# Kernel tuning notes

Measured on AMD Instinct MI355X. Metric: run time of the kernel, lower is better.

The kernel has to match this reference:

```python
import jax, jax.numpy as jnp
import numpy as np

N = 16384
E = 524288
D_IN = 256
D_OUT = 256


def setup_inputs() -> dict:
    key = jax.random.key(0)
    k1, k2, k3, k4, k5, k6 = jax.random.split(key, 6)
    x = jax.random.normal(k1, (N, D_IN), dtype=jnp.float32)
    edge_index = jax.random.randint(k2, (2, E), 0, N, dtype=jnp.int64)
    W_update = jax.random.normal(k3, (D_OUT, D_IN), dtype=jnp.float32) / np.sqrt(D_IN)
    b_update = jax.random.normal(k4, (D_OUT,), dtype=jnp.float32) * 0.01
    W_aggregate = jax.random.normal(k5, (D_OUT, D_IN), dtype=jnp.float32) / np.sqrt(D_IN)
    b_aggregate = jax.random.normal(k6, (D_OUT,), dtype=jnp.float32) * 0.01
    return {
        "x": x,
        "edge_index": edge_index,
        "W_update": W_update,
        "b_update": b_update,
        "W_aggregate": W_aggregate,
        "b_aggregate": b_aggregate,
    }


def reference(x, edge_index, W_update, b_update, W_aggregate, b_aggregate):
    n = x.shape[0]
    src, dst = edge_index[0], edge_index[1]
    # Dense symmetric 0/1 adjacency built with SET semantics (duplicate edges
    # contribute 1, not their count) -- faithful to the torch indexing assign.
    adj = jnp.zeros((n, n), dtype=x.dtype)
    adj = adj.at[src, dst].set(1.0)
    adj = adj.at[dst, src].set(1.0)
    messages = adj @ x                                   # [N, D_in]
    aggregated = messages @ W_aggregate.T + b_aggregate  # [N, D_out]
    updated = x @ W_update.T + b_update + aggregated     # [N, D_out]
    return updated
```

## Files before the change

### kernel.cpp

```cpp
#include <hip/hip_runtime.h>
#include <hip/hip_fp16.h>

#define NN 16384
#define DD 256
#define CAP 160
#define NB 128
#define BK 64
#define LDAP 72

typedef __attribute__((ext_vector_type(8))) __bf16 bf16x8;
typedef __attribute__((ext_vector_type(4))) float f32x4;

__device__ __forceinline__ unsigned short f2bn(float f) {
    __bf16 h = (__bf16)f;
    return __builtin_bit_cast(unsigned short, h);
}

__global__ __launch_bounds__(512) void k_hist(const int* __restrict__ ei,
                                              unsigned short* __restrict__ H,
                                              const float* __restrict__ Wu,
                                              const float* __restrict__ Wa,
                                              unsigned short* __restrict__ wb,
                                              int E, int epb) {
    const int b = blockIdx.x;
    const int t = threadIdx.x;

    if (b >= NB) {
        const int w = b - NB;
        const float* src = (w < 4) ? Wu : Wa;
        unsigned short* dst = wb + ((w < 4) ? 0 : 65536);
        const int c0 = (w & 3) * 4096;
#pragma unroll
        for (int i = 0; i < 8; ++i) {
            const int f4 = c0 + i * 512 + t;
            float4 v = *(const float4*)(src + (size_t)f4 * 4);
            ushort4 o;
            o.x = f2bn(v.x); o.y = f2bn(v.y); o.z = f2bn(v.z); o.w = f2bn(v.w);
            *(ushort4*)(dst + (size_t)f4 * 4) = o;
        }
        return;
    }

    __shared__ unsigned int h[NN / 2];
    for (int i = t; i < NN / 2; i += 512) h[i] = 0u;
    __syncthreads();

    const int e0 = b * epb;
    const int e1 = min(e0 + epb, E);
    for (int e = e0 + t; e < e1; e += 512) {
        const int s = ei[e];
        const int d = ei[E + e];
        atomicAdd(&h[s >> 1], 1u << ((s & 1) << 4));
        atomicAdd(&h[d >> 1], 1u << ((d & 1) << 4));
    }
    __syncthreads();

    unsigned short* Hb = H + (size_t)b * NN;
    for (int r = t; r < NN; r += 512)
        Hb[r] = (unsigned short)((h[r >> 1] >> ((r & 1) << 4)) & 0xffffu);
}

__global__ __launch_bounds__(512) void k_gemm_scan(const float* __restrict__ x,
                                                   const unsigned short* __restrict__ wb,
                                                   const float* __restrict__ bu,
                                                   const float* __restrict__ ba,
                                                   unsigned short* __restrict__ H,
                                                   unsigned int* __restrict__ cnt,
                                                   float* __restrict__ out,
                                                   __half* __restrict__ xab) {
    __shared__ __align__(16) unsigned short As[128 * LDAP];
    __shared__ __align__(16) unsigned short Bs[256 * LDAP];

    const int t = threadIdx.x;

    if (blockIdx.x >= 256) {
        const int r = (blockIdx.x - 256) * 512 + t;
        unsigned int base = 0;
#pragma unroll 8
        for (int bb = 0; bb < NB; ++bb) {
            const size_t a = (size_t)bb * NN + r;
            const unsigned int v = H[a];
            H[a] = (unsigned short)base;
            base += v;
        }
        cnt[r] = base;
        return;
    }

    const int lane = t & 63;
    const int wid = t >> 6;
    const int wr = wid >> 2;
    const int wc = wid & 3;
    const int row0 = (blockIdx.x >> 1) << 7;
    const int colp = blockIdx.x & 1;
    const unsigned short* Wsrc = wb + ((size_t)colp << 16);

    f32x4 acc[4][4] = {};

    for (int k0 = 0; k0 < DD; k0 += BK) {
        float4 ga[4];
        uint4 rb[4];
#pragma unroll
        for (int i = 0; i < 4; ++i) {
            const int ca = i * 512 + t;
            const int ar = ca >> 4, as = ca & 15;
            ga[i] = *(const float4*)(x + (size_t)(row0 + ar) * DD + k0 + as * 4);
            const int cb = i * 512 + t;
            const int br = cb >> 3, bs = cb & 7;
            rb[i] = *(const uint4*)(Wsrc + (size_t)br * DD + k0 + bs * 8);
        }
        __syncthreads();
#pragma unroll
        for (int i = 0; i < 4; ++i) {
            const int ca = i * 512 + t;
            const int ar = ca >> 4, as = ca & 15;
            ushort4 ap;
            ap.x = f2bn(ga[i].x); ap.y = f2bn(ga[i].y);
            ap.z = f2bn(ga[i].z); ap.w = f2bn(ga[i].w);
            *(ushort4*)(&As[ar * LDAP + as * 4]) = ap;
            const int cb = i * 512 + t;
            const int br = cb >> 3, bs = cb & 7;
            *(uint4*)(&Bs[br * LDAP + bs * 8]) = rb[i];
        }
        __syncthreads();
#pragma unroll
        for (int kk = 0; kk < 2; ++kk) {
            bf16x8 av[4], bv[4];
#pragma unroll
            for (int f = 0; f < 4; ++f) {
                uint4 ra = *(const uint4*)(&As[(wr * 64 + f * 16 + (lane & 15)) * LDAP + kk * 32 + (lane >> 4) * 8]);
                av[f] = __builtin_bit_cast(bf16x8, ra);
                uint4 rv = *(const uint4*)(&Bs[(wc * 64 + f * 16 + (lane & 15)) * LDAP + kk * 32 + (lane >> 4) * 8]);
                bv[f] = __builtin_bit_cast(bf16x8, rv);
            }
#pragma unroll
            for (int fm = 0; fm < 4; ++fm)
#pragma unroll
                for (int fn = 0; fn < 4; ++fn)
                    acc[fm][fn] = __builtin_amdgcn_mfma_f32_16x16x32_bf16(
                        av[fm], bv[fn], acc[fm][fn], 0, 0, 0);
        }
    }

    const int gr0 = row0 + wr * 64 + ((lane >> 4) << 2);
    const int gc0 = wc * 64 + (lane & 15);
    if (colp == 0) {
#pragma unroll
        for (int fn = 0; fn < 4; ++fn) {
            const int c = gc0 + fn * 16;
            const float bias = bu[c] + ba[c];
#pragma unroll
            for (int fm = 0; fm < 4; ++fm) {
                const int r = gr0 + fm * 16;
#pragma unroll
                for (int i = 0; i < 4; ++i)
                    out[(size_t)(r + i) * DD + c] = acc[fm][fn][i] + bias;
            }
        }
    } else {
#pragma unroll
        for (int fn = 0; fn < 4; ++fn) {
            const int c = gc0 + fn * 16;
#pragma unroll
            for (int fm = 0; fm < 4; ++fm) {
                const int r = gr0 + fm * 16;
#pragma unroll
                for (int i = 0; i < 4; ++i)
                    xab[(size_t)(r + i) * DD + c] = __float2half(acc[fm][fn][i]);
            }
        }
    }
}

__global__ __launch_bounds__(512) void k_fill(const int* __restrict__ ei,
                                              const unsigned short* __restrict__ H,
                                              unsigned short* __restrict__ list,
                                              int E, int epb) {
    __shared__ unsigned int off[NN / 2];
    const int b = blockIdx.x;
    const int t = threadIdx.x;
    for (int i = t; i < NN / 2; i += 512) off[i] = 0u;
    __syncthreads();

    const unsigned short* Hb = H + (size_t)b * NN;
    const int e0 = b * epb;
    const int e1 = min(e0 + epb, E);
    for (int e = e0 + t; e < e1; e += 512) {
        const int s = ei[e];
        const int d = ei[E + e];
        const int sh1 = (s & 1) << 4;
        const unsigned int o1 = atomicAdd(&off[s >> 1], 1u << sh1);
        const int p1 = (int)Hb[s] + (int)((o1 >> sh1) & 0xffffu);
        if (p1 < CAP) list[(size_t)s * CAP + p1] = (unsigned short)d;
        const int sh2 = (d & 1) << 4;
        const unsigned int o2 = atomicAdd(&off[d >> 1], 1u << sh2);
        const int p2 = (int)Hb[d] + (int)((o2 >> sh2) & 0xffffu);
        if (p2 < CAP) list[(size_t)d * CAP + p2] = (unsigned short)s;
    }
}

__global__ __launch_bounds__(256) void k_gather(const unsigned int* __restrict__ cnt,
                                                const unsigned short* __restrict__ list,
                                                const __half* __restrict__ xab,
                                                float* __restrict__ out) {
    __shared__ uint4 bmv[4][128];
    __shared__ unsigned short lst[4][CAP];

    const int t = threadIdx.x;
    const int wid = t >> 6;
    const int lane = t & 63;
    const int row = (blockIdx.x << 2) + wid;

    uint4 z; z.x = 0u; z.y = 0u; z.z = 0u; z.w = 0u;
    bmv[wid][lane] = z;
    bmv[wid][64 + lane] = z;
    const int m = min((int)cnt[row], CAP);
    __syncthreads();

    unsigned int* bw = (unsigned int*)&bmv[wid][0];
    const unsigned short* gl = list + (size_t)row * CAP;
    for (int i = lane; i < m; i += 64) {
        const int idx = gl[i];
        atomicOr(&bw[idx >> 5], 1u << (idx & 31));
    }
    __syncthreads();

    int base = 0;
#pragma unroll
    for (int g = 0; g < 2; ++g) {
        const int q = (g << 6) + lane;
        uint4 w = bmv[wid][q];
        int c = __popc(w.x) + __popc(w.y) + __popc(w.z) + __popc(w.w);
        int incl = c;
#pragma unroll
        for (int dd = 1; dd < 64; dd <<= 1) {
            int y = __shfl_up(incl, dd, 64);
            if (lane >= dd) incl += y;
        }
        int pos = base + incl - c;
        const int wbase = q << 7;
        unsigned int bb; int bit;
        bb = w.x; while (bb) { bit = __ffs(bb) - 1; bb &= bb - 1;
            if (pos < CAP) lst[wid][pos] = (unsigned short)(wbase + bit); ++pos; }
        bb = w.y; while (bb) { bit = __ffs(bb) - 1; bb &= bb - 1;
            if (pos < CAP) lst[wid][pos] = (unsigned short)(wbase + 32 + bit); ++pos; }
        bb = w.z; while (bb) { bit = __ffs(bb) - 1; bb &= bb - 1;
            if (pos < CAP) lst[wid][pos] = (unsigned short)(wbase + 64 + bit); ++pos; }
        bb = w.w; while (bb) { bit = __ffs(bb) - 1; bb &= bb - 1;
            if (pos < CAP) lst[wid][pos] = (unsigned short)(wbase + 96 + bit); ++pos; }
        base += __shfl(incl, 63, 64);
    }
    __syncthreads();

    const int n = min(base, CAP);
    const int coff = lane << 2;

    __half2 a0[8], a1[8];
    const __half2 z2 = __float2half2_rn(0.0f);
#pragma unroll
    for (int j = 0; j < 8; ++j) { a0[j] = z2; a1[j] = z2; }

    int i = 0;
    for (; i + 16 <= n; i += 16) {
        uint2 v[16];
#pragma unroll
        for (int j = 0; j < 16; ++j) {
            const int idx = lst[wid][i + j];
            v[j] = *(const uint2*)(xab + (((size_t)idx) << 8) + coff);
        }
#pragma unroll
        for (int j = 0; j < 16; ++j) {
            a0[j & 7] = __hadd2(a0[j & 7], __builtin_bit_cast(__half2, v[j].x));
            a1[j & 7] = __hadd2(a1[j & 7], __builtin_bit_cast(__half2, v[j].y));
        }
    }
    for (; i < n; ++i) {
        const int idx = lst[wid][i];
        uint2 v = *(const uint2*)(xab + (((size_t)idx) << 8) + coff);
        a0[0] = __hadd2(a0[0], __builtin_bit_cast(__half2, v.x));
        a1[0] = __hadd2(a1[0], __builtin_bit_cast(__half2, v.y));
    }

#pragma unroll
    for (int j = 1; j < 8; ++j) { a0[0] = __hadd2(a0[0], a0[j]); a1[0] = __hadd2(a1[0], a1[j]); }
    const float2 f0 = __half22float2(a0[0]);
    const float2 f1 = __half22float2(a1[0]);

    float4* po = (float4*)(out + (((size_t)row) << 8) + coff);
    float4 o = *po;
    o.x += f0.x; o.y += f0.y; o.z += f1.x; o.w += f1.y;
    *po = o;
}

extern "C" void kernel_launch(void* const* d_in, const int* in_sizes, int n_in,
                              void* d_out, int out_size, void* d_ws, size_t ws_size,
                              hipStream_t stream) {
    const float* x  = (const float*)d_in[0];
    const int*   ei = (const int*)d_in[1];
    const float* Wu = (const float*)d_in[2];
    const float* bu = (const float*)d_in[3];
    const float* Wa = (const float*)d_in[4];
    const float* ba = (const float*)d_in[5];
    float* out = (float*)d_out;

    const int E = in_sizes[1] / 2;
    const int epb = (E + NB - 1) / NB;

    char* ws = (char*)d_ws;
    __half* xab = (__half*)ws;
    unsigned short* wb = (unsigned short*)(ws + 8388608);
    unsigned short* H = (unsigned short*)(ws + 9437184);
    unsigned int* cnt = (unsigned int*)(ws + 13631488);
    unsigned short* list = (unsigned short*)(ws + 14680064);

    k_hist<<<NB + 8, 512, 0, stream>>>(ei, H, Wu, Wa, wb, E, epb);
    k_gemm_scan<<<288, 512, 0, stream>>>(x, wb, bu, ba, H, cnt, out, xab);
    k_fill<<<NB, 512, 0, stream>>>(ei, H, list, E, epb);
    k_gather<<<NN / 4, 256, 0, stream>>>(cnt, list, xab, out);
}
```

Before: 101.8 us.

## Split gather into two column-plane passes with plane-major fp16 layout

```diff
diff --git a/kernel.cpp b/kernel.cpp
--- a/kernel.cpp
+++ b/kernel.cpp
@@ -7,6 +7,7 @@
 #define NB 128
 #define BK 64
 #define LDAP 72
+#define PL 2097152
 
 typedef __attribute__((ext_vector_type(8))) __bf16 bf16x8;
 typedef __attribute__((ext_vector_type(4))) float f32x4;
@@ -161,12 +162,13 @@
 #pragma unroll
         for (int fn = 0; fn < 4; ++fn) {
             const int c = gc0 + fn * 16;
+            const size_t pbase = (size_t)(c >> 7) * PL + (c & 127);
 #pragma unroll
             for (int fm = 0; fm < 4; ++fm) {
                 const int r = gr0 + fm * 16;
 #pragma unroll
                 for (int i = 0; i < 4; ++i)
-                    xab[(size_t)(r + i) * DD + c] = __float2half(acc[fm][fn][i]);
+                    xab[pbase + (size_t)(r + i) * 128] = __float2half(acc[fm][fn][i]);
             }
         }
     }
@@ -199,10 +201,70 @@
     }
 }
 
-__global__ __launch_bounds__(256) void k_gather(const unsigned int* __restrict__ cnt,
-                                                const unsigned short* __restrict__ list,
-                                                const __half* __restrict__ xab,
-                                                float* __restrict__ out) {
+#define ACC4(S, V) { \
+    acc[S][0] = __hadd2(acc[S][0], __builtin_bit_cast(__half2, (V).x)); \
+    acc[S][1] = __hadd2(acc[S][1], __builtin_bit_cast(__half2, (V).y)); \
+    acc[S][2] = __hadd2(acc[S][2], __builtin_bit_cast(__half2, (V).z)); \
+    acc[S][3] = __hadd2(acc[S][3], __builtin_bit_cast(__half2, (V).w)); }
+
+__device__ __forceinline__ void gather_plane(const unsigned short* lst, int n,
+                                             const __half* __restrict__ plane,
+                                             float* __restrict__ out,
+                                             int row, int outoff, int lane) {
+    const int lg = lane >> 4;
+    const int li = lane & 15;
+    __half2 acc[4][4];
+    const __half2 z2 = __float2half2_rn(0.0f);
+#pragma unroll
+    for (int s = 0; s < 4; ++s) { acc[s][0] = z2; acc[s][1] = z2; acc[s][2] = z2; acc[s][3] = z2; }
+
+    int i = 0;
+    for (; i + 32 <= n; i += 32) {
+        uint4 v[8];
+#pragma unroll
+        for (int j = 0; j < 8; ++j)
+            v[j] = *(const uint4*)(plane + ((size_t)lst[i + j * 4 + lg] << 7) + li * 8);
+#pragma unroll
+        for (int j = 0; j < 8; ++j) ACC4(j & 3, v[j]);
+    }
+    for (; i + 4 <= n; i += 4) {
+        uint4 v = *(const uint4*)(plane + ((size_t)lst[i + lg] << 7) + li * 8);
+        ACC4(0, v);
+    }
+    if (i < n && lg < n - i) {
+        uint4 v = *(const uint4*)(plane + ((size_t)lst[i + lg] << 7) + li * 8);
+        ACC4(1, v);
+    }
+
+#pragma unroll
+    for (int k = 0; k < 4; ++k) {
+        acc[0][k] = __hadd2(acc[0][k], __hadd2(acc[1][k], __hadd2(acc[2][k], acc[3][k])));
+        int v = __builtin_bit_cast(int, acc[0][k]);
+        v = __shfl_xor(v, 16, 64);
+        acc[0][k] = __hadd2(acc[0][k], __builtin_bit_cast(__half2, v));
+        v = __builtin_bit_cast(int, acc[0][k]);
+        v = __shfl_xor(v, 32, 64);
+        acc[0][k] = __hadd2(acc[0][k], __builtin_bit_cast(__half2, v));
+    }
+
+    if (lg == 0) {
+        float4* po = (float4*)(out + (size_t)row * DD + outoff + li * 8);
+        float4 o0 = po[0], o1 = po[1];
+        float2 f;
+        f = __half22float2(acc[0][0]); o0.x += f.x; o0.y += f.y;
+        f = __half22float2(acc[0][1]); o0.z += f.x; o0.w += f.y;
+        f = __half22float2(acc[0][2]); o1.x += f.x; o1.y += f.y;
+        f = __half22float2(acc[0][3]); o1.z += f.x; o1.w += f.y;
+        po[0] = o0; po[1] = o1;
+    }
+}
+
+__global__ __launch_bounds__(256) void k_gatherA(const unsigned int* __restrict__ cnt,
+                                                 const unsigned short* __restrict__ list,
+                                                 unsigned short* __restrict__ nlist,
+                                                 unsigned int* __restrict__ ncnt,
+                                                 const __half* __restrict__ xab,
+                                                 float* __restrict__ out) {
     __shared__ uint4 bmv[4][128];
     __shared__ unsigned short lst[4][CAP];
 
@@ -253,43 +315,29 @@
     __syncthreads();
 
     const int n = min(base, CAP);
-    const int coff = lane << 2;
-
-    __half2 a0[8], a1[8];
-    const __half2 z2 = __float2half2_rn(0.0f);
-#pragma unroll
-    for (int j = 0; j < 8; ++j) { a0[j] = z2; a1[j] = z2; }
-
-    int i = 0;
-    for (; i + 16 <= n; i += 16) {
-        uint2 v[16];
-#pragma unroll
-        for (int j = 0; j < 16; ++j) {
-            const int idx = lst[wid][i + j];
-            v[j] = *(const uint2*)(xab + (((size_t)idx) << 8) + coff);
-        }
-#pragma unroll
-        for (int j = 0; j < 16; ++j) {
-            a0[j & 7] = __hadd2(a0[j & 7], __builtin_bit_cast(__half2, v[j].x));
-            a1[j & 7] = __hadd2(a1[j & 7], __builtin_bit_cast(__half2, v[j].y));
-        }
-    }
-    for (; i < n; ++i) {
-        const int idx = lst[wid][i];
-        uint2 v = *(const uint2*)(xab + (((size_t)idx) << 8) + coff);
-        a0[0] = __hadd2(a0[0], __builtin_bit_cast(__half2, v.x));
-        a1[0] = __hadd2(a1[0], __builtin_bit_cast(__half2, v.y));
-    }
-
-#pragma unroll
-    for (int j = 1; j < 8; ++j) { a0[0] = __hadd2(a0[0], a0[j]); a1[0] = __hadd2(a1[0], a1[j]); }
-    const float2 f0 = __half22float2(a0[0]);
-    const float2 f1 = __half22float2(a1[0]);
-
-    float4* po = (float4*)(out + (((size_t)row) << 8) + coff);
-    float4 o = *po;
-    o.x += f0.x; o.y += f0.y; o.z += f1.x; o.w += f1.y;
-    *po = o;
+    if (lane == 0) ncnt[row] = (unsigned int)n;
+    for (int i = lane; i < n; i += 64) nlist[(size_t)row * CAP + i] = lst[wid][i];
+
+    gather_plane(lst[wid], n, xab, out, row, 0, lane);
+}
+
+__global__ __launch_bounds__(256) void k_gatherB(const unsigned int* __restrict__ ncnt,
+                                                 const unsigned short* __restrict__ nlist,
+                                                 const __half* __restrict__ xab,
+                                                 float* __restrict__ out) {
+    __shared__ unsigned short lst[4][CAP];
+
+    const int t = threadIdx.x;
+    const int wid = t >> 6;
+    const int lane = t & 63;
+    const int row = (blockIdx.x << 2) + wid;
+
+    const int n = min((int)ncnt[row], CAP);
+    const unsigned short* gl = nlist + (size_t)row * CAP;
+    for (int i = lane; i < n; i += 64) lst[wid][i] = gl[i];
+    __syncthreads();
+
+    gather_plane(lst[wid], n, xab + PL, out, row, 128, lane);
 }
 
 extern "C" void kernel_launch(void* const* d_in, const int* in_sizes, int n_in,
@@ -312,9 +360,12 @@
     unsigned short* H = (unsigned short*)(ws + 9437184);
     unsigned int* cnt = (unsigned int*)(ws + 13631488);
     unsigned short* list = (unsigned short*)(ws + 14680064);
+    unsigned short* nlist = (unsigned short*)(ws + 19922944);
+    unsigned int* ncnt = (unsigned int*)(ws + 25165824);
 
     k_hist<<<NB + 8, 512, 0, stream>>>(ei, H, Wu, Wa, wb, E, epb);
     k_gemm_scan<<<288, 512, 0, stream>>>(x, wb, bu, ba, H, cnt, out, xab);
     k_fill<<<NB, 512, 0, stream>>>(ei, H, list, E, epb);
-    k_gather<<<NN / 4, 256, 0, stream>>>(cnt, list, xab, out);
-}
+    k_gatherA<<<NN / 4, 256, 0, stream>>>(cnt, list, nlist, ncnt, xab, out);
+    k_gatherB<<<NN / 4, 256, 0, stream>>>(ncnt, nlist, xab, out);
+}
```

After: 92.37 us. 1.1x faster.
